# Kernel optimization log

Hardware: AMD Instinct MI355X
Metric: run time of the kernel (lower is better)

Reference implementation:

```python
import jax, jax.numpy as jnp
import numpy as np

NUM_GRAPHS = 4096
EPS = 1e-6

def _ln(x, g, b):
    mu = jnp.mean(x, axis=-1, keepdims=True)
    var = jnp.mean(jnp.square(x - mu), axis=-1, keepdims=True)
    return (x - mu) * jax.lax.rsqrt(var + EPS) * g + b

def setup_inputs() -> dict:
    key = jax.random.key(0)
    ks = jax.random.split(key, 8)
    N, D, H, DRUG = 262144, 128, 8, 128
    feat = jax.random.normal(ks[0], (N, D), dtype=jnp.float32)
    batch = jnp.sort(jax.random.randint(ks[1], (N,), 0, NUM_GRAPHS)).astype(jnp.int64)
    def lin(k, fi, fo):
        lim = 1.0 / np.sqrt(fi)
        return jax.random.uniform(k, (fi, fo), jnp.float32, -lim, lim)
    return {
        'feat': feat, 'batch': batch,
        'W1': lin(ks[2], D, 64), 'b1': jnp.zeros((64,), jnp.float32),
        'g1': jnp.ones((64,), jnp.float32), 'beta1': jnp.zeros((64,), jnp.float32),
        'W2': lin(ks[3], 64, H), 'b2': jnp.zeros((H,), jnp.float32),
        'W3': lin(ks[4], H * D, D), 'b3': jnp.zeros((D,), jnp.float32),
        'g3': jnp.ones((D,), jnp.float32), 'beta3': jnp.zeros((D,), jnp.float32),
        'W4': lin(ks[5], D, DRUG), 'b4': jnp.zeros((DRUG,), jnp.float32),
        'g4': jnp.ones((DRUG,), jnp.float32), 'beta4': jnp.zeros((DRUG,), jnp.float32),
    }

def reference(feat, batch, W1, b1, g1, beta1, W2, b2, W3, b3, g3, beta3, W4, b4, g4, beta4):
    seg = batch.astype(jnp.int32)
    # ATFC: Linear -> LeakyReLU -> LayerNorm -> Linear
    h = jax.nn.leaky_relu(feat @ W1 + b1)
    h = _ln(h, g1, beta1)
    att = jnp.exp(h @ W2 + b2)                      # [N, H]
    # segment softmax normalization
    s = jax.ops.segment_sum(att, seg, num_segments=NUM_GRAPHS)  # [B, H]
    att = att / s[seg]
    # weighted aggregation: outer product + segment sum -> [B, H, D]
    out = jax.ops.segment_sum(att[:, :, None] * feat[:, None, :], seg, num_segments=NUM_GRAPHS)
    out = out.reshape(NUM_GRAPHS, -1)               # [B, H*D]
    # output block (dropout is identity in eval mode)
    o = _ln(jax.nn.leaky_relu(out @ W3 + b3), g3, beta3)
    o = _ln(jax.nn.leaky_relu(o @ W4 + b4), g4, beta4)
    return o
```

## Files before the change

kernel.cpp:

```cpp
#include <hip/hip_runtime.h>
#include <math.h>

#define NG 4096
#define NN 262144
#define D 128
#define M1 64
#define NH 8
#define GPB 8
#define EPS 1e-6f

typedef __attribute__((ext_vector_type(8))) short short8;
typedef __attribute__((ext_vector_type(4))) short short4v;
typedef __attribute__((ext_vector_type(4))) float f32x4;

__device__ inline float leaky(float x) { return x > 0.f ? x : 0.01f * x; }

__device__ inline short f2bf(float f) {
  union { float f; unsigned u; } v; v.f = f;
  unsigned r = (v.u + 0x7fffu + ((v.u >> 16) & 1u)) >> 16;
  return (short)r;
}
__device__ inline float bf2f(short s) {
  union { unsigned u; float f; } v;
  v.u = ((unsigned)(unsigned short)s) << 16;
  return v.f;
}

__global__ __launch_bounds__(256) void k0b_prep(
    const float* __restrict__ W3, const float* __restrict__ W4,
    const int* __restrict__ batch,
    short* __restrict__ W3T, short* __restrict__ W4T,
    int* __restrict__ starts) {
  __shared__ float tile[64][65];
  int b = blockIdx.x, t = threadIdx.x;
  if (b >= 36) {
    int g = (b - 36) * 256 + t;
    int lo = 0, hi = NN;
    while (lo < hi) {
      int mid = (lo + hi) >> 1;
      if (batch[mid] < g) lo = mid + 1; else hi = mid;
    }
    starts[g] = lo;
    if (g == 0) starts[NG] = NN;
    return;
  }
  const float* src; short* dst; int kt, nt, tkl;
  if (b < 32) { src = W3; dst = W3T; kt = b >> 1; nt = b & 1; tkl = 1024; }
  else        { src = W4; dst = W4T; kt = (b - 32) >> 1; nt = (b - 32) & 1; tkl = 128; }

#pragma unroll
  for (int i = 0; i < 4; ++i) {
    int id = t + 256 * i;
    int r = id >> 4, c4 = (id & 15) * 4;
    float4 v = *(const float4*)(src + (size_t)(kt * 64 + r) * D + nt * 64 + c4);
    tile[r][c4 + 0] = v.x; tile[r][c4 + 1] = v.y;
    tile[r][c4 + 2] = v.z; tile[r][c4 + 3] = v.w;
  }
  __syncthreads();
  int n = t >> 2, kb = (t & 3) * 16;
  short8 p0, p1;
#pragma unroll
  for (int j = 0; j < 8; ++j) {
    p0[j] = f2bf(tile[kb + j][n]);
    p1[j] = f2bf(tile[kb + 8 + j][n]);
  }
  short* o = dst + (size_t)(nt * 64 + n) * tkl + kt * 64 + kb;
  *(short8*)o = p0;
  *(short8*)(o + 8) = p1;
}

__global__ __launch_bounds__(256, 2) void kA_att(
    const float* __restrict__ feat, const int* __restrict__ batch,
    const float* __restrict__ W1, const float* __restrict__ b1,
    const float* __restrict__ g1, const float* __restrict__ beta1,
    const float* __restrict__ W2, const float* __restrict__ b2,
    short* __restrict__ attT, float* __restrict__ s_sum) {
  __shared__ __align__(16) short W1T[M1][D + 8];
  __shared__ __align__(16) short W2T[16][M1 + 8];
  __shared__ __align__(16) short hb[128][72];
  __shared__ __align__(16) short attB[NH][136];
  __shared__ int batchL[128];

  int t = threadIdx.x;
  int nb = blockIdx.x * 128;
  int w = t >> 6, l = t & 63;
  int lr = l & 15, lq = l >> 4;

#pragma unroll
  for (int i = 0; i < 8; ++i) {
    int idx4 = t + 256 * i;
    int k = idx4 >> 4, j = (idx4 & 15) * 4;
    float4 wv = *(const float4*)(W1 + k * M1 + j);
    W1T[j + 0][k] = f2bf(wv.x);
    W1T[j + 1][k] = f2bf(wv.y);
    W1T[j + 2][k] = f2bf(wv.z);
    W1T[j + 3][k] = f2bf(wv.w);
  }
#pragma unroll
  for (int i = 0; i < 4; ++i) {
    int e = t * 4 + i;
    int hh = e >> 6, j = e & 63;
    W2T[hh][j] = (hh < NH) ? f2bf(W2[j * NH + hh]) : (short)0;
  }
  if (t < 128) batchL[t] = batch[nb + t];

  float b1v[4], g1v[4], btv[4];
#pragma unroll
  for (int nt = 0; nt < 4; ++nt) {
    b1v[nt] = b1[nt * 16 + lr];
    g1v[nt] = g1[nt * 16 + lr];
    btv[nt] = beta1[nt * 16 + lr];
  }
  float b2v = b2[lr & 7];

  short8 afr[2][4];
#pragma unroll
  for (int mt = 0; mt < 2; ++mt) {
    const float* rp = feat + (size_t)(nb + w * 32 + mt * 16 + lr) * D + lq * 8;
#pragma unroll
    for (int cc = 0; cc < 4; ++cc) {
      float4 x0 = *(const float4*)(rp + cc * 32);
      float4 x1 = *(const float4*)(rp + cc * 32 + 4);
      short8 a;
      a[0] = f2bf(x0.x); a[1] = f2bf(x0.y); a[2] = f2bf(x0.z); a[3] = f2bf(x0.w);
      a[4] = f2bf(x1.x); a[5] = f2bf(x1.y); a[6] = f2bf(x1.z); a[7] = f2bf(x1.w);
      afr[mt][cc] = a;
    }
  }
  __syncthreads();

  f32x4 acc[2][4];
#pragma unroll
  for (int mt = 0; mt < 2; ++mt)
#pragma unroll
    for (int nt = 0; nt < 4; ++nt) acc[mt][nt] = (f32x4){0.f, 0.f, 0.f, 0.f};
  __builtin_amdgcn_s_setprio(1);
#pragma unroll
  for (int cc = 0; cc < 4; ++cc) {
#pragma unroll
    for (int nt = 0; nt < 4; ++nt) {
      short8 bfr = *(const short8*)&W1T[nt * 16 + lr][cc * 32 + lq * 8];
      acc[0][nt] = __builtin_amdgcn_mfma_f32_16x16x32_bf16(afr[0][cc], bfr, acc[0][nt], 0, 0, 0);
      acc[1][nt] = __builtin_amdgcn_mfma_f32_16x16x32_bf16(afr[1][cc], bfr, acc[1][nt], 0, 0, 0);
    }
  }
  __builtin_amdgcn_s_setprio(0);

#pragma unroll
  for (int mt = 0; mt < 2; ++mt) {
#pragma unroll
    for (int r = 0; r < 4; ++r) {
      float x[4], sa = 0.f, sb = 0.f;
#pragma unroll
      for (int nt = 0; nt < 4; ++nt) {
        float xvv = leaky(acc[mt][nt][r] + b1v[nt]);
        x[nt] = xvv; sa += xvv; sb = fmaf(xvv, xvv, sb);
      }
#pragma unroll
      for (int off = 1; off < 16; off <<= 1) {
        sa += __shfl_xor(sa, off);
        sb += __shfl_xor(sb, off);
      }
      float mu = sa * (1.f / M1);
      float var = sb * (1.f / M1) - mu * mu;
      float inv = rsqrtf(var + EPS);
      int node = w * 32 + mt * 16 + lq * 4 + r;
#pragma unroll
      for (int nt = 0; nt < 4; ++nt)
        hb[node][nt * 16 + lr] = f2bf((x[nt] - mu) * inv * g1v[nt] + btv[nt]);
    }
  }
  __syncthreads();

  f32x4 acc2[2];
  acc2[0] = (f32x4){0.f, 0.f, 0.f, 0.f};
  acc2[1] = (f32x4){0.f, 0.f, 0.f, 0.f};
#pragma unroll
  for (int c2 = 0; c2 < 2; ++c2) {
    short8 bfr2 = *(const short8*)&W2T[lr][c2 * 32 + lq * 8];
#pragma unroll
    for (int mt = 0; mt < 2; ++mt) {
      short8 af2 = *(const short8*)&hb[w * 32 + mt * 16 + lr][c2 * 32 + lq * 8];
      acc2[mt] = __builtin_amdgcn_mfma_f32_16x16x32_bf16(af2, bfr2, acc2[mt], 0, 0, 0);
    }
  }

  int g_lo = batchL[0], g_hi = batchL[127];

  if (lr < NH) {
    float attv[2][4];
    int bnode[2][4];
#pragma unroll
    for (int mt = 0; mt < 2; ++mt)
#pragma unroll
      for (int r = 0; r < 4; ++r) {
        int node = w * 32 + mt * 16 + lq * 4 + r;
        float av = bf2f(f2bf(expf(acc2[mt][r] + b2v)));
        attv[mt][r] = av;
        bnode[mt][r] = batchL[node];
        attB[lr][node] = f2bf(av);
      }
    for (int g = g_lo; g <= g_hi; ++g) {
      float ss = 0.f;
#pragma unroll
      for (int mt = 0; mt < 2; ++mt)
#pragma unroll
        for (int r = 0; r < 4; ++r)
          ss += (bnode[mt][r] == g) ? attv[mt][r] : 0.f;
      ss += __shfl_xor(ss, 16);
      ss += __shfl_xor(ss, 32);
      if (lq == 0) atomicAdd(s_sum + g * NH + lr, ss);
    }
  }
  __syncthreads();

  {
    int h = t >> 5, c4 = (t & 31) * 4;
    short4v v = *(const short4v*)&attB[h][c4];
    *(short4v*)(attT + (size_t)h * NN + nb + c4) = v;
  }
}

__global__ __launch_bounds__(256, 2) void kB_agg(
    const float* __restrict__ feat, const int* __restrict__ batch,
    const int* __restrict__ starts, const short* __restrict__ attT,
    const float* __restrict__ s_sum,
    const short* __restrict__ W3T, const float* __restrict__ b3,
    const float* __restrict__ g3, const float* __restrict__ beta3,
    const short* __restrict__ W4T, const float* __restrict__ b4,
    const float* __restrict__ g4, const float* __restrict__ beta4,
    float* __restrict__ out) {
  __shared__ __align__(16) short aLb[GPB][1040];
  __shared__ __align__(16) short hbuf2[16][136];
  __shared__ float red[4][2][16];
  __shared__ float sLb[GPB * NH];

  int t = threadIdx.x;
  int G0 = blockIdx.x * GPB;
  int w = t >> 6, l = t & 63;
  int lr = l & 15, lq = l >> 4;
  int dA = w * 32 + lr, dB = dA + 16;
  int hA = lr & 7;
  int laneoff = lr >> 3;

  int s0 = starts[G0], s1 = starts[G0 + GPB];
  int base0 = s0 & ~127;
  int nch = (s1 - base0 + 127) >> 7;

  f32x4 cc[4][2];
#pragma unroll
  for (int T = 0; T < 4; ++T) {
    cc[T][0] = (f32x4){0.f, 0.f, 0.f, 0.f};
    cc[T][1] = (f32x4){0.f, 0.f, 0.f, 0.f};
  }

  for (int c = 0; c < nch; ++c) {
    int base = base0 + (c << 7);
    int lo0 = batch[base];
    int hi0 = batch[min(base + 127, NN - 1)];
    if (hi0 < G0 || lo0 > G0 + GPB - 1) continue;
    bool fastp = (base + 128 <= NN);
#pragma unroll 1
    for (int kc = 0; kc < 4; ++kc) {
      int nb0 = base + kc * 32;
      int klo = batch[min(nb0, NN - 1)];
      int khi = batch[min(nb0 + 31, NN - 1)];
      if (khi < G0 || klo > G0 + GPB - 1) continue;
      int n0 = nb0 + lq * 8;
      short8 av;
      int bv[8];
      short8 bfa, bfb;
      if (fastp) {
        av = *(const short8*)(attT + (size_t)hA * NN + n0);
        int4 bx = *(const int4*)(batch + n0);
        int4 by = *(const int4*)(batch + n0 + 4);
        bv[0] = bx.x; bv[1] = bx.y; bv[2] = bx.z; bv[3] = bx.w;
        bv[4] = by.x; bv[5] = by.y; bv[6] = by.z; bv[7] = by.w;
#pragma unroll
        for (int j = 0; j < 8; ++j) {
          const float* fp = feat + (size_t)(n0 + j) * D;
          bfa[j] = f2bf(fp[dA]);
          bfb[j] = f2bf(fp[dB]);
        }
      } else {
#pragma unroll
        for (int j = 0; j < 8; ++j) {
          int n = min(n0 + j, NN - 1);
          av[j] = attT[(size_t)hA * NN + n];
          bv[j] = batch[n];
          const float* fp = feat + (size_t)n * D;
          bfa[j] = f2bf(fp[dA]);
          bfb[j] = f2bf(fp[dB]);
        }
      }
#pragma unroll
      for (int T = 0; T < 4; ++T) {
        int tg = G0 + 2 * T;
        if (khi < tg || klo > tg + 1) continue;
        int tgt = tg + laneoff;
        short8 am;
#pragma unroll
        for (int j = 0; j < 8; ++j) am[j] = (bv[j] == tgt) ? av[j] : (short)0;
        cc[T][0] = __builtin_amdgcn_mfma_f32_16x16x32_bf16(am, bfa, cc[T][0], 0, 0, 0);
        cc[T][1] = __builtin_amdgcn_mfma_f32_16x16x32_bf16(am, bfb, cc[T][1], 0, 0, 0);
      }
    }
  }

  if (t < GPB * NH) {
    float sv = s_sum[G0 * NH + t];
    sLb[t] = sv > 0.f ? 1.f / sv : 0.f;
  }
  __syncthreads();

#pragma unroll
  for (int T = 0; T < 4; ++T) {
    int gi = 2 * T + (lq >> 1);
    int hC = (lq & 1) * 4;
#pragma unroll
    for (int r = 0; r < 4; ++r) {
      float inv = sLb[gi * NH + hC + r];
      aLb[gi][(hC + r) * 128 + dA] = f2bf(cc[T][0][r] * inv);
      aLb[gi][(hC + r) * 128 + dB] = f2bf(cc[T][1][r] * inv);
    }
  }
  __syncthreads();

  int ar = lr & 7;
  f32x4 acc3[2];
  acc3[0] = (f32x4){0.f, 0.f, 0.f, 0.f};
  acc3[1] = (f32x4){0.f, 0.f, 0.f, 0.f};
#pragma unroll
  for (int kc = 0; kc < 32; ++kc) {
    short8 a = *(const short8*)&aLb[ar][kc * 32 + lq * 8];
#pragma unroll
    for (int nt = 0; nt < 2; ++nt) {
      int ncol = w * 32 + nt * 16 + lr;
      short8 b = *(const short8*)(W3T + (size_t)ncol * 1024 + kc * 32 + lq * 8);
      acc3[nt] = __builtin_amdgcn_mfma_f32_16x16x32_bf16(a, b, acc3[nt], 0, 0, 0);
    }
  }

  float xv[2][4], sa[4] = {0.f, 0.f, 0.f, 0.f}, sb[4] = {0.f, 0.f, 0.f, 0.f};
#pragma unroll
  for (int nt = 0; nt < 2; ++nt) {
    float bb = b3[w * 32 + nt * 16 + lr];
#pragma unroll
    for (int r = 0; r < 4; ++r) {
      float v = leaky(acc3[nt][r] + bb);
      xv[nt][r] = v;
      sa[r] += v;
      sb[r] = fmaf(v, v, sb[r]);
    }
  }
#pragma unroll
  for (int off = 1; off < 16; off <<= 1)
#pragma unroll
    for (int r = 0; r < 4; ++r) {
      sa[r] += __shfl_xor(sa[r], off);
      sb[r] += __shfl_xor(sb[r], off);
    }
  if (lr == 0)
#pragma unroll
    for (int r = 0; r < 4; ++r) {
      red[w][0][lq * 4 + r] = sa[r];
      red[w][1][lq * 4 + r] = sb[r];
    }
  __syncthreads();
#pragma unroll
  for (int nt = 0; nt < 2; ++nt) {
    int col = w * 32 + nt * 16 + lr;
    float gg = g3[col], bt = beta3[col];
#pragma unroll
    for (int r = 0; r < 4; ++r) {
      int row = lq * 4 + r;
      float S1 = red[0][0][row] + red[1][0][row] + red[2][0][row] + red[3][0][row];
      float S2 = red[0][1][row] + red[1][1][row] + red[2][1][row] + red[3][1][row];
      float mu = S1 * (1.f / D);
      float var = S2 * (1.f / D) - mu * mu;
      float inv = rsqrtf(var + EPS);
      hbuf2[row][col] = f2bf((xv[nt][r] - mu) * inv * gg + bt);
    }
  }
  __syncthreads();

  f32x4 acc4[2];
  acc4[0] = (f32x4){0.f, 0.f, 0.f, 0.f};
  acc4[1] = (f32x4){0.f, 0.f, 0.f, 0.f};
#pragma unroll
  for (int kc = 0; kc < 4; ++kc) {
    short8 a2 = *(const short8*)&hbuf2[lr][kc * 32 + lq * 8];
#pragma unroll
    for (int nt = 0; nt < 2; ++nt) {
      int ncol = w * 32 + nt * 16 + lr;
      short8 b4f = *(const short8*)(W4T + (size_t)ncol * 128 + kc * 32 + lq * 8);
      acc4[nt] = __builtin_amdgcn_mfma_f32_16x16x32_bf16(a2, b4f, acc4[nt], 0, 0, 0);
    }
  }
#pragma unroll
  for (int r = 0; r < 4; ++r) { sa[r] = 0.f; sb[r] = 0.f; }
#pragma unroll
  for (int nt = 0; nt < 2; ++nt) {
    float bb = b4[w * 32 + nt * 16 + lr];
#pragma unroll
    for (int r = 0; r < 4; ++r) {
      float v = leaky(acc4[nt][r] + bb);
      xv[nt][r] = v;
      sa[r] += v;
      sb[r] = fmaf(v, v, sb[r]);
    }
  }
#pragma unroll
  for (int off = 1; off < 16; off <<= 1)
#pragma unroll
    for (int r = 0; r < 4; ++r) {
      sa[r] += __shfl_xor(sa[r], off);
      sb[r] += __shfl_xor(sb[r], off);
    }
  __syncthreads();
  if (lr == 0)
#pragma unroll
    for (int r = 0; r < 4; ++r) {
      red[w][0][lq * 4 + r] = sa[r];
      red[w][1][lq * 4 + r] = sb[r];
    }
  __syncthreads();
#pragma unroll
  for (int nt = 0; nt < 2; ++nt) {
    int col = w * 32 + nt * 16 + lr;
    float gg = g4[col], bt = beta4[col];
#pragma unroll
    for (int r = 0; r < 4; ++r) {
      int row = lq * 4 + r;
      if (row < GPB) {
        float S1 = red[0][0][row] + red[1][0][row] + red[2][0][row] + red[3][0][row];
        float S2 = red[0][1][row] + red[1][1][row] + red[2][1][row] + red[3][1][row];
        float mu = S1 * (1.f / D);
        float var = S2 * (1.f / D) - mu * mu;
        float inv = rsqrtf(var + EPS);
        out[(size_t)(G0 + row) * D + col] = (xv[nt][r] - mu) * inv * gg + bt;
      }
    }
  }
}

extern "C" void kernel_launch(void* const* d_in, const int* in_sizes, int n_in,
                              void* d_out, int out_size, void* d_ws, size_t ws_size,
                              hipStream_t stream) {
  (void)in_sizes; (void)n_in; (void)out_size; (void)ws_size;
  const float* feat  = (const float*)d_in[0];
  const int*   batch = (const int*)d_in[1];
  const float* W1    = (const float*)d_in[2];
  const float* b1    = (const float*)d_in[3];
  const float* g1    = (const float*)d_in[4];
  const float* beta1 = (const float*)d_in[5];
  const float* W2    = (const float*)d_in[6];
  const float* b2    = (const float*)d_in[7];
  const float* W3    = (const float*)d_in[8];
  const float* b3    = (const float*)d_in[9];
  const float* g3    = (const float*)d_in[10];
  const float* beta3 = (const float*)d_in[11];
  const float* W4    = (const float*)d_in[12];
  const float* b4    = (const float*)d_in[13];
  const float* g4    = (const float*)d_in[14];
  const float* beta4 = (const float*)d_in[15];
  float* out = (float*)d_out;

  char* ws = (char*)d_ws;
  short* W3T    = (short*)ws;
  short* W4T    = (short*)(ws + 262144);
  int*   starts = (int*)(ws + 294912);
  float* s_sum  = (float*)(ws + 311552);
  short* attT   = (short*)(ws + 442624);

  hipMemsetAsync(s_sum, 0, (size_t)NG * NH * 4, stream);
  k0b_prep<<<52, 256, 0, stream>>>(W3, W4, batch, W3T, W4T, starts);
  kA_att<<<NN / 128, 256, 0, stream>>>(feat, batch, W1, b1, g1, beta1, W2, b2,
                                       attT, s_sum);
  kB_agg<<<NG / GPB, 256, 0, stream>>>(feat, batch, starts, attT, s_sum, W3T,
                                       b3, g3, beta3, W4T, b4, g4, beta4, out);
}
```

Measured before the change: 279.6 us.

## Halve graphs per aggregation block, fold s_sum memset into prep, alias LDS

Graphs per aggregation block drop from 8 to 4, doubling the block count so more CUs share the gather and output-MLP work, at the cost of re-reading W3T/W4T in more blocks. The separate hipMemsetAsync of s_sum becomes 16 extra blocks in the prep kernel, removing one launch. In the attention kernel, W1T and hb now share one LDS union with an added barrier, cutting LDS per block and possibly raising occupancy.

New measurement: 292.7 us. 4.7% more time.

```diff
diff --git a/kernel.cpp b/kernel.cpp
--- a/kernel.cpp
+++ b/kernel.cpp
@@ -6,7 +6,7 @@
 #define D 128
 #define M1 64
 #define NH 8
-#define GPB 8
+#define GPB 4
 #define EPS 1e-6f
 
 typedef __attribute__((ext_vector_type(8))) short short8;
@@ -30,9 +30,16 @@
     const float* __restrict__ W3, const float* __restrict__ W4,
     const int* __restrict__ batch,
     short* __restrict__ W3T, short* __restrict__ W4T,
-    int* __restrict__ starts) {
+    int* __restrict__ starts, float* __restrict__ s_sum) {
   __shared__ float tile[64][65];
   int b = blockIdx.x, t = threadIdx.x;
+  if (b >= 52) {
+    float4 z = (float4){0.f, 0.f, 0.f, 0.f};
+    float* p = s_sum + ((size_t)(b - 52) * 256 + t) * 8;
+    *(float4*)p = z;
+    *(float4*)(p + 4) = z;
+    return;
+  }
   if (b >= 36) {
     int g = (b - 36) * 256 + t;
     int lo = 0, hi = NN;
@@ -75,9 +82,11 @@
     const float* __restrict__ g1, const float* __restrict__ beta1,
     const float* __restrict__ W2, const float* __restrict__ b2,
     short* __restrict__ attT, float* __restrict__ s_sum) {
-  __shared__ __align__(16) short W1T[M1][D + 8];
+  __shared__ __align__(16) union UA {
+    short W1T[M1][D + 8];
+    short hb[128][68];
+  } ua;
   __shared__ __align__(16) short W2T[16][M1 + 8];
-  __shared__ __align__(16) short hb[128][72];
   __shared__ __align__(16) short attB[NH][136];
   __shared__ int batchL[128];
 
@@ -91,10 +100,10 @@
     int idx4 = t + 256 * i;
     int k = idx4 >> 4, j = (idx4 & 15) * 4;
     float4 wv = *(const float4*)(W1 + k * M1 + j);
-    W1T[j + 0][k] = f2bf(wv.x);
-    W1T[j + 1][k] = f2bf(wv.y);
-    W1T[j + 2][k] = f2bf(wv.z);
-    W1T[j + 3][k] = f2bf(wv.w);
+    ua.W1T[j + 0][k] = f2bf(wv.x);
+    ua.W1T[j + 1][k] = f2bf(wv.y);
+    ua.W1T[j + 2][k] = f2bf(wv.z);
+    ua.W1T[j + 3][k] = f2bf(wv.w);
   }
 #pragma unroll
   for (int i = 0; i < 4; ++i) {
@@ -139,12 +148,13 @@
   for (int cc = 0; cc < 4; ++cc) {
 #pragma unroll
     for (int nt = 0; nt < 4; ++nt) {
-      short8 bfr = *(const short8*)&W1T[nt * 16 + lr][cc * 32 + lq * 8];
+      short8 bfr = *(const short8*)&ua.W1T[nt * 16 + lr][cc * 32 + lq * 8];
       acc[0][nt] = __builtin_amdgcn_mfma_f32_16x16x32_bf16(afr[0][cc], bfr, acc[0][nt], 0, 0, 0);
       acc[1][nt] = __builtin_amdgcn_mfma_f32_16x16x32_bf16(afr[1][cc], bfr, acc[1][nt], 0, 0, 0);
     }
   }
   __builtin_amdgcn_s_setprio(0);
+  __syncthreads();
 
 #pragma unroll
   for (int mt = 0; mt < 2; ++mt) {
@@ -167,7 +177,7 @@
       int node = w * 32 + mt * 16 + lq * 4 + r;
 #pragma unroll
       for (int nt = 0; nt < 4; ++nt)
-        hb[node][nt * 16 + lr] = f2bf((x[nt] - mu) * inv * g1v[nt] + btv[nt]);
+        ua.hb[node][nt * 16 + lr] = f2bf((x[nt] - mu) * inv * g1v[nt] + btv[nt]);
     }
   }
   __syncthreads();
@@ -180,7 +190,7 @@
     short8 bfr2 = *(const short8*)&W2T[lr][c2 * 32 + lq * 8];
 #pragma unroll
     for (int mt = 0; mt < 2; ++mt) {
-      short8 af2 = *(const short8*)&hb[w * 32 + mt * 16 + lr][c2 * 32 + lq * 8];
+      short8 af2 = *(const short8*)&ua.hb[w * 32 + mt * 16 + lr][c2 * 32 + lq * 8];
       acc2[mt] = __builtin_amdgcn_mfma_f32_16x16x32_bf16(af2, bfr2, acc2[mt], 0, 0, 0);
     }
   }
@@ -247,9 +257,9 @@
   int base0 = s0 & ~127;
   int nch = (s1 - base0 + 127) >> 7;
 
-  f32x4 cc[4][2];
-#pragma unroll
-  for (int T = 0; T < 4; ++T) {
+  f32x4 cc[2][2];
+#pragma unroll
+  for (int T = 0; T < 2; ++T) {
     cc[T][0] = (f32x4){0.f, 0.f, 0.f, 0.f};
     cc[T][1] = (f32x4){0.f, 0.f, 0.f, 0.f};
   }
@@ -294,7 +304,7 @@
         }
       }
 #pragma unroll
-      for (int T = 0; T < 4; ++T) {
+      for (int T = 0; T < 2; ++T) {
         int tg = G0 + 2 * T;
         if (khi < tg || klo > tg + 1) continue;
         int tgt = tg + laneoff;
@@ -314,7 +324,7 @@
   __syncthreads();
 
 #pragma unroll
-  for (int T = 0; T < 4; ++T) {
+  for (int T = 0; T < 2; ++T) {
     int gi = 2 * T + (lq >> 1);
     int hC = (lq & 1) * 4;
 #pragma unroll
@@ -326,7 +336,7 @@
   }
   __syncthreads();
 
-  int ar = lr & 7;
+  int ar = lr & (GPB - 1);
   f32x4 acc3[2];
   acc3[0] = (f32x4){0.f, 0.f, 0.f, 0.f};
   acc3[1] = (f32x4){0.f, 0.f, 0.f, 0.f};
@@ -473,8 +483,7 @@
   float* s_sum  = (float*)(ws + 311552);
   short* attT   = (short*)(ws + 442624);
 
-  hipMemsetAsync(s_sum, 0, (size_t)NG * NH * 4, stream);
-  k0b_prep<<<52, 256, 0, stream>>>(W3, W4, batch, W3T, W4T, starts);
+  k0b_prep<<<68, 256, 0, stream>>>(W3, W4, batch, W3T, W4T, starts, s_sum);
   kA_att<<<NN / 128, 256, 0, stream>>>(feat, batch, W1, b1, g1, beta1, W2, b2,
                                        attT, s_sum);
   kB_agg<<<NG / GPB, 256, 0, stream>>>(feat, batch, starts, attT, s_sum, W3T,
```
